# Kernel tuning notes

Measured on AMD Instinct MI355X. Metric: run time of the kernel, lower is better.

Reference implementation:

```python
import jax, jax.numpy as jnp
from jax import lax
import numpy as np

# Config mirroring init_kwargs
B, N, PD = 4, 16384, 3
PROJ = 64                 # projection_channel
M1, K1, C1 = 2048, 32, 128  # level-1 SA: fps points, neighbors, out channel
M2, K2, C2 = 512, 32, 256   # level-2 SA
DH, DO = 512, 256           # dense hidden / out (dense_channels)


def fps(pts, M):
    """Farthest point sampling. pts: [N,3] -> indices [M] (starts at point 0)."""
    n = pts.shape[0]
    def step(carry, _):
        dmin, last = carry
        d = jnp.sum((pts - pts[last]) ** 2, axis=-1)   # dist to newest center
        dmin = jnp.minimum(dmin, d)
        nxt = jnp.argmax(dmin).astype(jnp.int32)
        return (dmin, nxt), last
    init = (jnp.full((n,), 1e10, pts.dtype), jnp.int32(0))
    _, idxs = lax.scan(step, init, None, length=M)
    return idxs


def sa_level(pts, feats, M, K, Wa, ba, Wb, bb):
    """PointNet++ set abstraction: FPS + kNN (xyz space) + grouped MLP + max."""
    idx = jax.vmap(lambda p: fps(p, M))(pts)                       # [B,M]
    centers = jnp.take_along_axis(pts, idx[:, :, None], axis=1)    # [B,M,3]
    d = jnp.sum((centers[:, :, None, :] - pts[:, None, :, :]) ** 2, -1)  # [B,M,N]
    _, nidx = lax.top_k(-d, K)                                      # [B,M,K]
    gather = jax.vmap(lambda a, i: a[i])
    rel = gather(pts, nidx) - centers[:, :, None, :]                # [B,M,K,3]
    nf = gather(feats, nidx)                                        # [B,M,K,C]
    g = jnp.concatenate([rel, nf], axis=-1)                         # use_xyz=True
    h = jax.nn.relu(g @ Wa + ba)
    h = jax.nn.relu(h @ Wb + bb)
    return centers, jnp.max(h, axis=2)                              # [B,M,Cout]


def setup_inputs() -> dict:
    key = jax.random.key(0)
    ks = jax.random.split(key, 12)
    w = lambda k, shape, s: jax.random.normal(k, shape, jnp.float32) * s
    z = lambda c: jnp.zeros((c,), jnp.float32)
    return {
        "xyz": jax.random.normal(ks[0], (B, N, PD), jnp.float32),
        "Wp": w(ks[1], (PD, PROJ), 0.3), "bp": z(PROJ),
        "W1a": w(ks[2], (PROJ + 3, C1), 0.1), "b1a": z(C1),
        "W1b": w(ks[3], (C1, C1), 0.08), "b1b": z(C1),
        "W2a": w(ks[4], (C1 + 3, C2), 0.08), "b2a": z(C2),
        "W2b": w(ks[5], (C2, C2), 0.06), "b2b": z(C2),
        "Wd1": w(ks[6], (2 * C2, DH), 0.05), "bd1": z(DH),
        "Wd2": w(ks[7], (DH, DO), 0.05), "bd2": z(DO),
    }


def reference(xyz, Wp, bp, W1a, b1a, W1b, b1b, W2a, b2a, W2b, b2b,
              Wd1, bd1, Wd2, bd2):
    feats = xyz @ Wp + bp            # point_proj: [B,N,PROJ]
    pts = xyz[..., :3]
    pts, feats = sa_level(pts, feats, M1, K1, W1a, b1a, W1b, b1b)
    pts, feats = sa_level(pts, feats, M2, K2, W2a, b2a, W2b, b2b)
    # global max + avg pool (adaptive_max/avg_pool1d to 1), concat -> [B,2*C2]
    g = jnp.concatenate([jnp.max(feats, axis=1), jnp.mean(feats, axis=1)], -1)
    h = jax.nn.relu(g @ Wd1 + bd1)   # DenseBlock w/ activation
    return h @ Wd2 + bd2             # last block: no activation (last_activation=False)
```

## Files before the change

### kernel.cpp

```cpp
#include <hip/hip_runtime.h>

#define B_    4
#define N1_   16384
#define M1_   2048
#define M2_   512
#define KNN_  32
#define PROJ_ 64
#define C1_   128
#define C2_   256
#define PROJ_OFF_  4
#define TAIL1_OFF_ (PROJ_OFF_ + 8192)
#define TAIL2_OFF_ (TAIL1_OFF_ + 32 * 512)
#define HEAD_OFF_  (TAIL2_OFF_ + 8 * 512)
#define TOTAL_BLKS_ (HEAD_OFF_ + B_)

__device__ __forceinline__ float sqdist_exact(float px, float py, float pz,
                                              float cx, float cy, float cz) {
    float dx = __fsub_rn(px, cx);
    float dy = __fsub_rn(py, cy);
    float dz = __fsub_rn(pz, cz);
    return __fadd_rn(__fadd_rn(__fmul_rn(dx, dx), __fmul_rn(dy, dy)), __fmul_rn(dz, dz));
}

__device__ __forceinline__ float aload(const float* p) {
    return __uint_as_float(__hip_atomic_load((const unsigned*)p,
                           __ATOMIC_RELAXED, __HIP_MEMORY_SCOPE_AGENT));
}
__device__ __forceinline__ unsigned auload(const unsigned* p) {
    return __hip_atomic_load(p, __ATOMIC_RELAXED, __HIP_MEMORY_SCOPE_AGENT);
}
__device__ __forceinline__ void afence() {
    __builtin_amdgcn_fence(__ATOMIC_ACQUIRE, "agent");
}

#define F_PROG1(f,b)  ((f) + (b) * 16)
#define F_PROG2(f,b)  ((f) + 64 + (b) * 16)
#define F_PROJD(f)    ((f) + 128)
#define F_K1D(f,b,c)  ((f) + 192 + ((b) * 32 + (c)) * 16)
#define F_M2D(f,b)    ((f) + 2240 + (b) * 16)
#define F_K2D(f,b,c)  ((f) + 2304 + ((b) * 8 + (c)) * 16)
#define F_M1D(f,b)    ((f) + 2816 + (b) * 16)

__global__ void __launch_bounds__(1024)
sortx_kernel(const float* __restrict__ xyz, float* __restrict__ sx,
             float* __restrict__ sy, float* __restrict__ sz,
             float* __restrict__ sp) {
    const int b = blockIdx.x, t = threadIdx.x;
    const int lane = t & 63, w = t >> 6;
    const float* P = xyz + (size_t)b * N1_ * 3;
    __shared__ int hist[1024];
    __shared__ int wsum[16];
    hist[t] = 0;
    __syncthreads();
    for (int j = t; j < N1_; j += 1024) {
        unsigned kb = __float_as_uint(P[j * 3]);
        kb ^= (kb >> 31) ? 0xFFFFFFFFu : 0x80000000u;
        atomicAdd(&hist[kb >> 22], 1);
    }
    __syncthreads();
    int v = hist[t];
    int cum = v;
    for (int off = 1; off < 64; off <<= 1) {
        int o = __shfl_up(cum, off);
        if (lane >= off) cum += o;
    }
    if (lane == 63) wsum[w] = cum;
    __syncthreads();
    int wpre = 0;
    for (int i = 0; i < w; ++i) wpre += wsum[i];
    const int excl = cum - v + wpre;
    __syncthreads();
    hist[t] = excl;
    __syncthreads();
    for (int j = t; j < N1_; j += 1024) {
        float x = P[j * 3], y = P[j * 3 + 1], z = P[j * 3 + 2];
        unsigned kb = __float_as_uint(x);
        kb ^= (kb >> 31) ? 0xFFFFFFFFu : 0x80000000u;
        int pos = atomicAdd(&hist[kb >> 22], 1);
        size_t o = (size_t)b * N1_ + pos;
        sx[o] = x; sy[o] = y; sz[o] = z;
        float* pr = sp + ((size_t)b * N1_ + pos) * 3;
        pr[0] = x; pr[1] = y; pr[2] = z;
    }
}

typedef float v2f __attribute__((ext_vector_type(2)));

template<int CTRL, int RM>
__device__ __forceinline__ unsigned long long dpp_umax64(unsigned long long pk) {
    unsigned lo = (unsigned)__builtin_amdgcn_update_dpp(
        0, (int)(unsigned)pk, CTRL, RM, 0xf, true);
    unsigned hi = (unsigned)__builtin_amdgcn_update_dpp(
        0, (int)(unsigned)(pk >> 32), CTRL, RM, 0xf, true);
    unsigned long long o = ((unsigned long long)hi << 32) | (unsigned long long)lo;
    return (o > pk) ? o : pk;
}

__device__ __forceinline__ unsigned long long wave_max_key(unsigned long long pk) {
    pk = dpp_umax64<0x111, 0xf>(pk);
    pk = dpp_umax64<0x112, 0xf>(pk);
    pk = dpp_umax64<0x114, 0xf>(pk);
    pk = dpp_umax64<0x118, 0xf>(pk);
    pk = dpp_umax64<0x142, 0xa>(pk);
    pk = dpp_umax64<0x143, 0xc>(pk);
    return pk;
}

__device__ __forceinline__ unsigned reduce8_widx(const unsigned long long* wk,
                                                 int lane) {
    unsigned long long k8 = wk[lane & 7];
    k8 = dpp_umax64<0x111, 0xf>(k8);
    k8 = dpp_umax64<0x112, 0xf>(k8);
    k8 = dpp_umax64<0x114, 0xf>(k8);
    unsigned lo = (unsigned)__builtin_amdgcn_readlane((int)(unsigned)k8, 7);
    return ~lo;
}

template<int N, int NT>
__device__ void knn_bodyT(const float* __restrict__ P,
                          float cx, float cy, float cz,
                          int* __restrict__ out, char* arena) {
    constexpr int K = KNN_;
    constexpr int CAP = 224;
    const int t = threadIdx.x;
    const int lane = t & 63;
    const int w = t >> 6;

    int*      hist = (int*)arena;
    unsigned* eqk  = (unsigned*)(arena + 8192);
    int*      eqi  = (int*)(arena + 8192 + 896);
    int*      wsum = (int*)(arena + 8192 + 1792);
    int*      ctrl = (int*)(arena + 8192 + 1824);

    unsigned prefix = 0; int pbits = 0;
    unsigned Tlo = 0; unsigned long long Thi = 0x100000000ull;
    int L = 0, target = K, Cbin = N;

    for (int round = 0; round < 3; ++round) {
        const int bits  = (round < 2) ? 11 : 10;
        const int nbins = 1 << bits;
        const int shift = 32 - pbits - bits;
        for (int i = t; i < nbins; i += NT) hist[i] = 0;
        __syncthreads();
        for (int j = t; j < N; j += NT) {
            float d = sqdist_exact(P[j * 3], P[j * 3 + 1], P[j * 3 + 2], cx, cy, cz);
            unsigned key = __float_as_uint(d);
            if (key >= Tlo && (unsigned long long)key < Thi)
                atomicAdd(&hist[(key >> shift) & (nbins - 1)], 1);
        }
        __syncthreads();
        const int per = nbins / NT;
        int s = 0;
        for (int i = 0; i < per; ++i) s += hist[t * per + i];
        int cum = s;
        for (int off = 1; off < 64; off <<= 1) {
            int o = __shfl_up(cum, off);
            if (lane >= off) cum += o;
        }
        if (lane == 63) wsum[w] = cum;
        __syncthreads();
        int wpre = 0;
        for (int i = 0; i < w; ++i) wpre += wsum[i];
        cum += wpre;
        const int cumex = cum - s;
        if ((cumex < target) && (cum >= target)) {
            int acc = cumex;
            for (int i = 0; i < per; ++i) {
                int h = hist[t * per + i];
                if (acc + h >= target) { ctrl[2] = t * per + i; ctrl[3] = acc; ctrl[4] = h; break; }
                acc += h;
            }
        }
        __syncthreads();
        const int binsel = ctrl[2];
        const int Ladd   = ctrl[3];
        const int bincnt = ctrl[4];
        L += Ladd;
        target -= Ladd;
        prefix = (prefix << bits) | (unsigned)binsel;
        pbits += bits;
        Tlo = prefix << (32 - pbits);
        Thi = ((unsigned long long)prefix + 1ull) << (32 - pbits);
        Cbin = bincnt;
        __syncthreads();
        if (Cbin <= CAP) break;
    }

    if (t == 0) { ctrl[0] = 0; ctrl[1] = 0; }
    __syncthreads();

    if (Cbin <= CAP) {
        for (int j = t; j < N; j += NT) {
            float d = sqdist_exact(P[j * 3], P[j * 3 + 1], P[j * 3 + 2], cx, cy, cz);
            unsigned key = __float_as_uint(d);
            if (key < Tlo) {
                int p = atomicAdd(&ctrl[0], 1);
                out[p] = j;
            } else if ((unsigned long long)key < Thi) {
                int p = atomicAdd(&ctrl[1], 1);
                eqk[p] = key; eqi[p] = j;
            }
        }
        __syncthreads();
        const int E = ctrl[1];
        for (int e = t; e < E; e += NT) {
            unsigned ke = eqk[e]; int ie = eqi[e];
            int rank = 0;
            for (int f = 0; f < E; ++f) {
                unsigned kf = eqk[f]; int jf = eqi[f];
                rank += (kf < ke || (kf == ke && jf < ie)) ? 1 : 0;
            }
            if (rank < target) out[L + rank] = ie;
        }
    } else {
        if (t < 64) {
            int cnt = 0;
            for (int jb = 0; jb < N; jb += 64) {
                int j = jb + lane;
                float d = sqdist_exact(P[j * 3], P[j * 3 + 1], P[j * 3 + 2], cx, cy, cz);
                unsigned key = __float_as_uint(d);
                if (key < Tlo) {
                    int p = atomicAdd(&ctrl[0], 1);
                    out[p] = j;
                }
                bool eq = (key == Tlo);
                unsigned long long mb = __ballot(eq);
                int below = __popcll(mb & ((1ull << lane) - 1ull));
                if (eq && (cnt + below) < target) out[L + cnt + below] = j;
                cnt += (int)__popcll(mb);
            }
        }
    }
}

__device__ void mlp1_512(int b, int m, char* arena,
                         const float* __restrict__ xyz,
                         const float* __restrict__ feats0,
                         const float* __restrict__ centers1,
                         const int* __restrict__ nidx1,
                         const float* __restrict__ Wa, const float* __restrict__ ba,
                         const float* __restrict__ Wb, const float* __restrict__ bb,
                         float* __restrict__ feats1) {
    constexpr int KN = KNN_, FD = PROJ_, CO = C1_, GS = FD + 4;
    const int t = threadIdx.x;
    const size_t bm = (size_t)b * M1_ + m;
    float (*g)[GS]  = (float(*)[GS])arena;
    float (*h1)[CO] = (float(*)[CO])(arena + 8704);
    float (*pm)[CO] = (float(*)[CO])(arena + 8704 + 16384);
    const int* nb = nidx1 + bm * KN;
    const float* cen = centers1 + bm * 3;
    const float cx = cen[0], cy = cen[1], cz = cen[2];
    {
        const int kk = t >> 4;
        const int q  = t & 15;
        const int j  = nb[kk];
        const float* f = feats0 + ((size_t)b * N1_ + j) * FD + q * 4;
        *(float4*)&g[kk][q * 4] = *(const float4*)f;
        if (q == 0) {
            const float* p = xyz + ((size_t)b * N1_ + j) * 3;
            g[kk][FD + 0] = __fsub_rn(p[0], cx);
            g[kk][FD + 1] = __fsub_rn(p[1], cy);
            g[kk][FD + 2] = __fsub_rn(p[2], cz);
            g[kk][FD + 3] = 0.f;
        }
    }
    __syncthreads();
    const int o = t & (CO - 1);
    const int grp = t >> 7;
    const int k0 = grp * 8;
    float acc[8];
#pragma unroll
    for (int k = 0; k < 8; ++k) acc[k] = ba[o];
    for (int s4 = 0; s4 < FD / 4; ++s4) {
        const float w0 = Wa[(4 * s4 + 3) * CO + o];
        const float w1 = Wa[(4 * s4 + 4) * CO + o];
        const float w2 = Wa[(4 * s4 + 5) * CO + o];
        const float w3 = Wa[(4 * s4 + 6) * CO + o];
#pragma unroll
        for (int k = 0; k < 8; ++k) {
            float4 gv = *(const float4*)&g[k0 + k][4 * s4];
            acc[k] = __fmaf_rn(gv.x, w0, acc[k]);
            acc[k] = __fmaf_rn(gv.y, w1, acc[k]);
            acc[k] = __fmaf_rn(gv.z, w2, acc[k]);
            acc[k] = __fmaf_rn(gv.w, w3, acc[k]);
        }
    }
    {
        const float w0 = Wa[0 * CO + o];
        const float w1 = Wa[1 * CO + o];
        const float w2 = Wa[2 * CO + o];
#pragma unroll
        for (int k = 0; k < 8; ++k) {
            float4 gv = *(const float4*)&g[k0 + k][FD];
            acc[k] = __fmaf_rn(gv.x, w0, acc[k]);
            acc[k] = __fmaf_rn(gv.y, w1, acc[k]);
            acc[k] = __fmaf_rn(gv.z, w2, acc[k]);
        }
    }
#pragma unroll
    for (int k = 0; k < 8; ++k) h1[k0 + k][o] = fmaxf(acc[k], 0.f);
    __syncthreads();
#pragma unroll
    for (int k = 0; k < 8; ++k) acc[k] = bb[o];
    for (int s4 = 0; s4 < CO / 4; ++s4) {
        const float w0 = Wb[(4 * s4 + 0) * CO + o];
        const float w1 = Wb[(4 * s4 + 1) * CO + o];
        const float w2 = Wb[(4 * s4 + 2) * CO + o];
        const float w3 = Wb[(4 * s4 + 3) * CO + o];
#pragma unroll
        for (int k = 0; k < 8; ++k) {
            float4 hv = *(const float4*)&h1[k0 + k][4 * s4];
            acc[k] = __fmaf_rn(hv.x, w0, acc[k]);
            acc[k] = __fmaf_rn(hv.y, w1, acc[k]);
            acc[k] = __fmaf_rn(hv.z, w2, acc[k]);
            acc[k] = __fmaf_rn(hv.w, w3, acc[k]);
        }
    }
    float mx = 0.f;
#pragma unroll
    for (int k = 0; k < 8; ++k) mx = fmaxf(mx, fmaxf(acc[k], 0.f));
    pm[grp][o] = mx;
    __syncthreads();
    if (t < CO) {
        float m0 = fmaxf(fmaxf(pm[0][o], pm[1][o]), fmaxf(pm[2][o], pm[3][o]));
        feats1[bm * CO + o] = m0;
    }
}

__device__ void mlp2_512(int b, int m, char* arena,
                         const float* __restrict__ centers1,
                         const float* __restrict__ feats1,
                         const float* __restrict__ centers2,
                         const int* __restrict__ nidx2,
                         const float* __restrict__ Wa, const float* __restrict__ ba,
                         const float* __restrict__ Wb, const float* __restrict__ bb,
                         float* __restrict__ feats2) {
    constexpr int KN = KNN_, FD = C1_, CO = C2_, GS = FD + 4;
    const int t = threadIdx.x;
    const size_t bm = (size_t)b * M2_ + m;
    float (*g)[GS]  = (float(*)[GS])arena;
    float (*h1)[CO] = (float(*)[CO])(arena + 16896);
    float (*pm)[CO] = (float(*)[CO])(arena + 16896 + 32768);
    const int* nb = nidx2 + bm * KN;
    const float* cen = centers2 + bm * 3;
    const float cx = cen[0], cy = cen[1], cz = cen[2];
    {
        const int kk = t >> 4;
        const int q  = t & 15;
        const int j  = nb[kk];
        const float* f = feats1 + ((size_t)b * M1_ + j) * FD + q * 8;
        *(float4*)&g[kk][q * 8]     = *(const float4*)f;
        *(float4*)&g[kk][q * 8 + 4] = *(const float4*)(f + 4);
        if (q == 0) {
            const float* p = centers1 + ((size_t)b * M1_ + j) * 3;
            g[kk][FD + 0] = __fsub_rn(p[0], cx);
            g[kk][FD + 1] = __fsub_rn(p[1], cy);
            g[kk][FD + 2] = __fsub_rn(p[2], cz);
            g[kk][FD + 3] = 0.f;
        }
    }
    __syncthreads();
    const int o = t & (CO - 1);
    const int grp = t >> 8;
    const int k0 = grp * 16;
    float acc[16];
#pragma unroll
    for (int k = 0; k < 16; ++k) acc[k] = ba[o];
    for (int s4 = 0; s4 < FD / 4; ++s4) {
        const float w0 = Wa[(4 * s4 + 3) * CO + o];
        const float w1 = Wa[(4 * s4 + 4) * CO + o];
        const float w2 = Wa[(4 * s4 + 5) * CO + o];
        const float w3 = Wa[(4 * s4 + 6) * CO + o];
#pragma unroll
        for (int k = 0; k < 16; ++k) {
            float4 gv = *(const float4*)&g[k0 + k][4 * s4];
            acc[k] = __fmaf_rn(gv.x, w0, acc[k]);
            acc[k] = __fmaf_rn(gv.y, w1, acc[k]);
            acc[k] = __fmaf_rn(gv.z, w2, acc[k]);
            acc[k] = __fmaf_rn(gv.w, w3, acc[k]);
        }
    }
    {
        const float w0 = Wa[0 * CO + o];
        const float w1 = Wa[1 * CO + o];
        const float w2 = Wa[2 * CO + o];
#pragma unroll
        for (int k = 0; k < 16; ++k) {
            float4 gv = *(const float4*)&g[k0 + k][FD];
            acc[k] = __fmaf_rn(gv.x, w0, acc[k]);
            acc[k] = __fmaf_rn(gv.y, w1, acc[k]);
            acc[k] = __fmaf_rn(gv.z, w2, acc[k]);
        }
    }
#pragma unroll
    for (int k = 0; k < 16; ++k) h1[k0 + k][o] = fmaxf(acc[k], 0.f);
    __syncthreads();
#pragma unroll
    for (int k = 0; k < 16; ++k) acc[k] = bb[o];
    for (int s4 = 0; s4 < CO / 4; ++s4) {
        const float w0 = Wb[(4 * s4 + 0) * CO + o];
        const float w1 = Wb[(4 * s4 + 1) * CO + o];
        const float w2 = Wb[(4 * s4 + 2) * CO + o];
        const float w3 = Wb[(4 * s4 + 3) * CO + o];
#pragma unroll
        for (int k = 0; k < 16; ++k) {
            float4 hv = *(const float4*)&h1[k0 + k][4 * s4];
            acc[k] = __fmaf_rn(hv.x, w0, acc[k]);
            acc[k] = __fmaf_rn(hv.y, w1, acc[k]);
            acc[k] = __fmaf_rn(hv.z, w2, acc[k]);
            acc[k] = __fmaf_rn(hv.w, w3, acc[k]);
        }
    }
    float mx = 0.f;
#pragma unroll
    for (int k = 0; k < 16; ++k) mx = fmaxf(mx, fmaxf(acc[k], 0.f));
    pm[grp][o] = mx;
    __syncthreads();
    if (t < CO) {
        feats2[bm * CO + o] = fmaxf(pm[0][o], pm[1][o]);
    }
}

__global__ __attribute__((amdgpu_flat_work_group_size(512, 512)))
__attribute__((amdgpu_waves_per_eu(2, 2)))
void mega_kernel(const float* __restrict__ xyz,
                 const float* __restrict__ sx, const float* __restrict__ sy,
                 const float* __restrict__ sz, const float* __restrict__ sp,
                 const float* __restrict__ Wp, const float* __restrict__ bp,
                 const float* __restrict__ W1a, const float* __restrict__ b1a,
                 const float* __restrict__ W1b, const float* __restrict__ b1b,
                 const float* __restrict__ W2a, const float* __restrict__ b2a,
                 const float* __restrict__ W2b, const float* __restrict__ b2b,
                 const float* __restrict__ Wd1, const float* __restrict__ bd1,
                 const float* __restrict__ Wd2, const float* __restrict__ bd2,
                 float* __restrict__ feats0, float* __restrict__ centers1,
                 int* __restrict__ nidx1, float* __restrict__ feats1,
                 float* __restrict__ centers2, int* __restrict__ nidx2,
                 float* __restrict__ feats2, float* __restrict__ outp,
                 unsigned* __restrict__ flags) {
#pragma clang fp contract(off)
    __shared__ alignas(16) char arena[51712];
    asm volatile("" ::: "v255");
    const int bid = blockIdx.x;
    const int t = threadIdx.x;

    if (bid >= HEAD_OFF_) {
        const int b = bid - HEAD_OFF_;
        if (t == 0) {
            while (auload(F_M2D(flags, b)) < (unsigned)M2_)
                __builtin_amdgcn_s_sleep(16);
        }
        __syncthreads();
        afence();
        float* gsh = (float*)arena;
        float* hsh = (float*)(arena + 2048);
        const float* F = feats2 + (size_t)b * M2_ * C2_;
        if (t < C2_) {
            float mx = -1e30f, sm = 0.f;
            for (int r = 0; r < M2_; ++r) {
                float v = F[r * C2_ + t];
                mx = fmaxf(mx, v);
                sm += v;
            }
            gsh[t] = mx;
            gsh[C2_ + t] = sm * (1.0f / (float)M2_);
        }
        __syncthreads();
        if (t < C2_) {
#pragma unroll
            for (int oo = 0; oo < 2; ++oo) {
                const int o = t + oo * 256;
                float acc = bd1[o];
                for (int i = 0; i < 512; ++i)
                    acc = __fmaf_rn(gsh[i], Wd1[i * 512 + o], acc);
                hsh[o] = fmaxf(acc, 0.f);
            }
        }
        __syncthreads();
        if (t < C2_) {
            float acc = bd2[t];
            for (int i = 0; i < 512; ++i)
                acc = __fmaf_rn(hsh[i], Wd2[i * 256 + t], acc);
            outp[b * 256 + t] = acc;
        }
        return;
    }
    if (bid >= TAIL2_OFF_) {
        const int k = bid - TAIL2_OFF_;
        const int c = k >> 9;
        const int r = k & 511;
        const int i = r & 255;
        const int b = (i >> 6) & 3;
        const int m = c * 64 + (i & 63);
        if (r < 256) {
            if (t == 0) {
                while (auload(F_PROG2(flags, b)) <= (unsigned)c)
                    __builtin_amdgcn_s_sleep(16);
            }
            __syncthreads();
            afence();
            const float* cw = centers2 + ((size_t)b * M2_ + m) * 3;
            float cx = cw[0], cy = cw[1], cz = cw[2];
            knn_bodyT<M1_, 512>(centers1 + (size_t)b * M1_ * 3, cx, cy, cz,
                                nidx2 + ((size_t)b * M2_ + m) * KNN_, arena);
            __syncthreads();
            if (t == 0)
                __hip_atomic_fetch_add(F_K2D(flags, b, c), 1u,
                                       __ATOMIC_RELEASE, __HIP_MEMORY_SCOPE_AGENT);
            return;
        }
        if (t == 0) {
            while (auload(F_K2D(flags, b, c)) < 64u ||
                   auload(F_M1D(flags, b)) < (unsigned)M1_)
                __builtin_amdgcn_s_sleep(16);
        }
        __syncthreads();
        afence();
        mlp2_512(b, m, arena, centers1, feats1, centers2, nidx2,
                 W2a, b2a, W2b, b2b, feats2);
        __syncthreads();
        if (t == 0)
            __hip_atomic_fetch_add(F_M2D(flags, b), 1u,
                                   __ATOMIC_RELEASE, __HIP_MEMORY_SCOPE_AGENT);
        return;
    }
    if (bid >= TAIL1_OFF_) {
        const int k = bid - TAIL1_OFF_;
        const int c = k >> 9;
        const int r = k & 511;
        const int i = r & 255;
        const int b = (i >> 6) & 3;
        const int m = c * 64 + (i & 63);
        if (r < 256) {
            if (t == 0) {
                while (auload(F_PROG1(flags, b)) <= (unsigned)c)
                    __builtin_amdgcn_s_sleep(16);
            }
            __syncthreads();
            const float* cw = centers1 + ((size_t)b * M1_ + m) * 3;
            float cx = aload(cw + 0), cy = aload(cw + 1), cz = aload(cw + 2);
            knn_bodyT<N1_, 512>(xyz + (size_t)b * N1_ * 3, cx, cy, cz,
                                nidx1 + ((size_t)b * M1_ + m) * KNN_, arena);
            __syncthreads();
            if (t == 0)
                __hip_atomic_fetch_add(F_K1D(flags, b, c), 1u,
                                       __ATOMIC_RELEASE, __HIP_MEMORY_SCOPE_AGENT);
            return;
        }
        if (t == 0) {
            while (auload(F_K1D(flags, b, c)) < 64u ||
                   auload(F_PROJD(flags)) < 8192u)
                __builtin_amdgcn_s_sleep(16);
        }
        __syncthreads();
        afence();
        mlp1_512(b, m, arena, xyz, feats0, centers1, nidx1,
                 W1a, b1a, W1b, b1b, feats1);
        __syncthreads();
        if (t == 0)
            __hip_atomic_fetch_add(F_M1D(flags, b), 1u,
                                   __ATOMIC_RELEASE, __HIP_MEMORY_SCOPE_AGENT);
        return;
    }
    if (bid >= B_) {
        int tid = (bid - B_) * 512 + t;
        int cc = tid & (PROJ_ - 1);
        int pn = tid >> 6;
        const float* p = xyz + (size_t)pn * 3;
        float acc = p[0] * Wp[0 * PROJ_ + cc];
        acc = __fmaf_rn(p[1], Wp[1 * PROJ_ + cc], acc);
        acc = __fmaf_rn(p[2], Wp[2 * PROJ_ + cc], acc);
        feats0[tid] = acc + bp[cc];
        __syncthreads();
        if (t == 0)
            __hip_atomic_fetch_add(F_PROJD(flags), 1u,
                                   __ATOMIC_RELEASE, __HIP_MEMORY_SCOPE_AGENT);
        return;
    }
    constexpr int NT = 512;
    constexpr int NW = NT / 64;
    const int b = bid;
    const int w = t >> 6;
    const int lane = t & 63;
    const float* P  = xyz + (size_t)b * N1_ * 3;
    const float* SX = sx + (size_t)b * N1_;
    const float* SY = sy + (size_t)b * N1_;
    const float* SZ = sz + (size_t)b * N1_;
    const float* SP = sp + (size_t)b * N1_ * 3;
    float* C1 = centers1 + (size_t)b * M1_ * 3;
    float* C2 = centers2 + (size_t)b * M2_ * 3;

    unsigned long long (*wkey)[NW] = (unsigned long long(*)[NW])arena;
    float* cb1 = (float*)(arena + 128);
    float* cb2 = (float*)(arena + 24704);

    {
        constexpr int PPT = N1_ / NT;
        const int base = t * PPT;
        const unsigned nbase = ~(unsigned)base;

        float px[PPT], py[PPT], pz[PPT], dmin[PPT];
#pragma unroll
        for (int k = 0; k < PPT; ++k) {
            px[k] = SX[base + k];
            py[k] = SY[base + k];
            pz[k] = SZ[base + k];
            dmin[k] = 1e10f;
        }
#pragma unroll
        for (int k = 0; k < PPT; ++k)
            asm volatile("" : "+v"(px[k]), "+v"(py[k]), "+v"(pz[k]), "+v"(dmin[k]));

        float xlo = px[0], xhi = px[0];
#pragma unroll
        for (int k = 1; k < PPT; ++k) {
            xlo = fminf(xlo, px[k]);
            xhi = fmaxf(xhi, px[k]);
        }
        for (int off = 1; off < 64; off <<= 1) {
            xlo = fminf(xlo, __shfl_xor(xlo, off));
            xhi = fmaxf(xhi, __shfl_xor(xhi, off));
        }

        unsigned long long mykey = ((unsigned long long)__float_as_uint(1e10f) << 32);
        float cx = P[0], cy = P[1], cz = P[2];

        for (int m = 0; m < M1_; ++m) {
            if (t == 0) {
                cb1[m * 3 + 0] = cx; cb1[m * 3 + 1] = cy; cb1[m * 3 + 2] = cz;
            }
            if ((m & 63) == 63) {
                __syncthreads();
                const int c = m >> 6;
                if (t < 48)
                    ((float4*)C1)[c * 48 + t] = ((const float4*)cb1)[c * 48 + t];
                __syncthreads();
                if (t == 0)
                    __hip_atomic_store(F_PROG1(flags, b), (unsigned)(c + 1),
                                       __ATOMIC_RELEASE, __HIP_MEMORY_SCOPE_AGENT);
            }
            if (m == M1_ - 1) break;
            const int par = m & 1;
            const float UBval = __uint_as_float((unsigned)(mykey >> 32));
            const float dxs = fmaxf(fmaxf(xlo - cx, cx - xhi), 0.0f);
            if (!(0.999f * (dxs * dxs) >= UBval)) {
                unsigned long long pk = 0;
#pragma unroll
                for (int k = 0; k < PPT; ++k) {
                    float d  = sqdist_exact(px[k], py[k], pz[k], cx, cy, cz);
                    float nd = fminf(dmin[k], d);
                    dmin[k] = nd;
                    unsigned long long kk =
                        ((unsigned long long)__float_as_uint(nd) << 32) |
                        (unsigned)(nbase - (unsigned)k);
                    pk = (kk > pk) ? kk : pk;
                }
                pk = wave_max_key(pk);
                unsigned klo = (unsigned)__builtin_amdgcn_readlane((int)(unsigned)pk, 63);
                unsigned khi = (unsigned)__builtin_amdgcn_readlane((int)(unsigned)(pk >> 32), 63);
                mykey = ((unsigned long long)khi << 32) | klo;
            }
            if (lane == 63) wkey[par][w] = mykey;
            __syncthreads();
            const unsigned widx = reduce8_widx(wkey[par], lane);
            const float* cp = SP + (size_t)widx * 3;
            cx = cp[0]; cy = cp[1]; cz = cp[2];
        }
    }
    __syncthreads();
    {
        constexpr int NP = (M1_ / NT) / 2;
        v2f px2[NP], py2[NP], pz2[NP];
        float dmin[2 * NP];
#pragma unroll
        for (int p = 0; p < NP; ++p) {
            const int j0 = (2 * p) * NT + t;
            const int j1 = j0 + NT;
            px2[p] = (v2f){cb1[j0 * 3 + 0], cb1[j1 * 3 + 0]};
            py2[p] = (v2f){cb1[j0 * 3 + 1], cb1[j1 * 3 + 1]};
            pz2[p] = (v2f){cb1[j0 * 3 + 2], cb1[j1 * 3 + 2]};
            dmin[2 * p] = 1e10f; dmin[2 * p + 1] = 1e10f;
        }
#pragma unroll
        for (int p = 0; p < NP; ++p)
            asm volatile("" : "+v"(px2[p]), "+v"(py2[p]), "+v"(pz2[p]));

        float cx = cb1[0], cy = cb1[1], cz = cb1[2];

        for (int m = 0; m < M2_; ++m) {
            if (t == 0) {
                cb2[m * 3 + 0] = cx; cb2[m * 3 + 1] = cy; cb2[m * 3 + 2] = cz;
            }
            if ((m & 63) == 63) {
                __syncthreads();
                const int c = m >> 6;
                if (t < 48)
                    ((float4*)C2)[c * 48 + t] = ((const float4*)cb2)[c * 48 + t];
                __syncthreads();
                if (t == 0)
                    __hip_atomic_store(F_PROG2(flags, b), (unsigned)(c + 1),
                                       __ATOMIC_RELEASE, __HIP_MEMORY_SCOPE_AGENT);
            }
            if (m == M2_ - 1) break;
            const int par = m & 1;
            const v2f c2x = {cx, cx}, c2y = {cy, cy}, c2z = {cz, cz};
            float bv = -1.0f; int bk = 0;
#pragma unroll
            for (int p = 0; p < NP; ++p) {
                v2f dx = px2[p] - c2x;
                v2f dy = py2[p] - c2y;
                v2f dz = pz2[p] - c2z;
                v2f d2 = (dx * dx + dy * dy) + dz * dz;
                float nd0 = fminf(dmin[2 * p],     d2.x);
                float nd1 = fminf(dmin[2 * p + 1], d2.y);
                dmin[2 * p]     = nd0;
                dmin[2 * p + 1] = nd1;
                bool g0 = nd0 > bv; bv = g0 ? nd0 : bv; bk = g0 ? 2 * p     : bk;
                bool g1 = nd1 > bv; bv = g1 ? nd1 : bv; bk = g1 ? 2 * p + 1 : bk;
            }
            unsigned gi = (unsigned)(bk * NT + t);
            unsigned long long pk =
                ((unsigned long long)__float_as_uint(bv) << 32) | (unsigned)(~gi);
            pk = wave_max_key(pk);
            if (lane == 63) wkey[par][w] = pk;
            __syncthreads();
            const unsigned widx = reduce8_widx(wkey[par], lane);
            cx = cb1[widx * 3 + 0];
            cy = cb1[widx * 3 + 1];
            cz = cb1[widx * 3 + 2];
        }
    }
}

extern "C" void kernel_launch(void* const* d_in, const int* in_sizes, int n_in,
                              void* d_out, int out_size, void* d_ws, size_t ws_size,
                              hipStream_t stream) {
    const float* xyz = (const float*)d_in[0];
    const float* Wp  = (const float*)d_in[1];
    const float* bp  = (const float*)d_in[2];
    const float* W1a = (const float*)d_in[3];
    const float* b1a = (const float*)d_in[4];
    const float* W1b = (const float*)d_in[5];
    const float* b1b = (const float*)d_in[6];
    const float* W2a = (const float*)d_in[7];
    const float* b2a = (const float*)d_in[8];
    const float* W2b = (const float*)d_in[9];
    const float* b2b = (const float*)d_in[10];
    const float* Wd1 = (const float*)d_in[11];
    const float* bd1 = (const float*)d_in[12];
    const float* Wd2 = (const float*)d_in[13];
    const float* bd2 = (const float*)d_in[14];
    float* out = (float*)d_out;

    char* ws = (char*)d_ws;
    size_t off = 0;
    auto alloc = [&](size_t bytes) { void* p = ws + off; off += (bytes + 255) & ~(size_t)255; return p; };
    float* feats0   = (float*)alloc((size_t)B_ * N1_ * PROJ_ * 4);
    float* centers1 = (float*)alloc((size_t)B_ * M1_ * 3 * 4);
    int*   nidx1    = (int*)  alloc((size_t)B_ * M1_ * KNN_ * 4);
    float* feats1   = (float*)alloc((size_t)B_ * M1_ * C1_ * 4);
    float* centers2 = (float*)alloc((size_t)B_ * M2_ * 3 * 4);
    int*   nidx2    = (int*)  alloc((size_t)B_ * M2_ * KNN_ * 4);
    float* feats2   = (float*)alloc((size_t)B_ * M2_ * C2_ * 4);
    unsigned* flags = (unsigned*)alloc(16384);
    float* sx       = (float*)alloc((size_t)B_ * N1_ * 4);
    float* sy       = (float*)alloc((size_t)B_ * N1_ * 4);
    float* sz       = (float*)alloc((size_t)B_ * N1_ * 4);
    float* sp       = (float*)alloc((size_t)B_ * N1_ * 3 * 4);
    (void)in_sizes; (void)n_in; (void)out_size; (void)ws_size;

    hipMemsetAsync(flags, 0, 16384, stream);

    sortx_kernel<<<dim3(B_), dim3(1024), 0, stream>>>(xyz, sx, sy, sz, sp);
    mega_kernel<<<dim3(TOTAL_BLKS_), dim3(512), 0, stream>>>(
        xyz, sx, sy, sz, sp, Wp, bp, W1a, b1a, W1b, b1b,
        W2a, b2a, W2b, b2b, Wd1, bd1, Wd2, bd2,
        feats0, centers1, nidx1, feats1, centers2, nidx2, feats2, out, flags);
}
```

Before: 3.252 ms.

## Split persistent mega-kernel into separate level-1 and level-2 kernels

Breaks the single flag-synchronised mega kernel into one kernel for level-1 FPS, projection, kNN and MLP, and a second kernel for level-2 FPS, kNN, MLP and the dense head. The level-2 FPS now reads centers from global memory after a kernel boundary instead of continuing in the same block from shared memory, and the M1-done flag wait is dropped. Level 1 gets a smaller shared-memory arena, which may allow more resident blocks. The cost is that level-2 FPS can no longer overlap with the level-1 MLP tail, and there is an extra launch.

```diff
diff --git a/kernel.cpp b/kernel.cpp
--- a/kernel.cpp
+++ b/kernel.cpp
@@ -8,11 +8,11 @@
 #define PROJ_ 64
 #define C1_   128
 #define C2_   256
-#define PROJ_OFF_  4
-#define TAIL1_OFF_ (PROJ_OFF_ + 8192)
-#define TAIL2_OFF_ (TAIL1_OFF_ + 32 * 512)
-#define HEAD_OFF_  (TAIL2_OFF_ + 8 * 512)
-#define TOTAL_BLKS_ (HEAD_OFF_ + B_)
+#define PROJ_BLKS_ ((B_ * N1_ * PROJ_) / 512)
+#define TAIL_BLKS_ (32 * 512)
+#define SA2_TAIL_OFF_ 4
+#define SA2_HEAD_OFF_ (SA2_TAIL_OFF_ + 8 * 512)
+#define SA2_BLKS_     (SA2_HEAD_OFF_ + B_)
 
 __device__ __forceinline__ float sqdist_exact(float px, float py, float pz,
                                               float cx, float cy, float cz) {
@@ -39,7 +39,6 @@
 #define F_K1D(f,b,c)  ((f) + 192 + ((b) * 32 + (c)) * 16)
 #define F_M2D(f,b)    ((f) + 2240 + (b) * 16)
 #define F_K2D(f,b,c)  ((f) + 2304 + ((b) * 8 + (c)) * 16)
-#define F_M1D(f,b)    ((f) + 2816 + (b) * 16)
 
 __global__ void __launch_bounds__(1024)
 sortx_kernel(const float* __restrict__ xyz, float* __restrict__ sx,
@@ -423,29 +422,173 @@
 
 __global__ __attribute__((amdgpu_flat_work_group_size(512, 512)))
 __attribute__((amdgpu_waves_per_eu(2, 2)))
-void mega_kernel(const float* __restrict__ xyz,
-                 const float* __restrict__ sx, const float* __restrict__ sy,
-                 const float* __restrict__ sz, const float* __restrict__ sp,
-                 const float* __restrict__ Wp, const float* __restrict__ bp,
-                 const float* __restrict__ W1a, const float* __restrict__ b1a,
-                 const float* __restrict__ W1b, const float* __restrict__ b1b,
-                 const float* __restrict__ W2a, const float* __restrict__ b2a,
-                 const float* __restrict__ W2b, const float* __restrict__ b2b,
-                 const float* __restrict__ Wd1, const float* __restrict__ bd1,
-                 const float* __restrict__ Wd2, const float* __restrict__ bd2,
-                 float* __restrict__ feats0, float* __restrict__ centers1,
-                 int* __restrict__ nidx1, float* __restrict__ feats1,
-                 float* __restrict__ centers2, int* __restrict__ nidx2,
-                 float* __restrict__ feats2, float* __restrict__ outp,
-                 unsigned* __restrict__ flags) {
+void mega1_kernel(const float* __restrict__ xyz,
+                  const float* __restrict__ sx, const float* __restrict__ sy,
+                  const float* __restrict__ sz, const float* __restrict__ sp,
+                  const float* __restrict__ Wp, const float* __restrict__ bp,
+                  const float* __restrict__ W1a, const float* __restrict__ b1a,
+                  const float* __restrict__ W1b, const float* __restrict__ b1b,
+                  float* __restrict__ feats0, float* __restrict__ centers1,
+                  int* __restrict__ nidx1, float* __restrict__ feats1,
+                  unsigned* __restrict__ flags) {
 #pragma clang fp contract(off)
-    __shared__ alignas(16) char arena[51712];
+    __shared__ alignas(16) char arena[27136];
     asm volatile("" ::: "v255");
     const int bid = blockIdx.x;
     const int t = threadIdx.x;
 
-    if (bid >= HEAD_OFF_) {
-        const int b = bid - HEAD_OFF_;
+    if (bid >= B_ + PROJ_BLKS_) {
+        const int k = bid - (B_ + PROJ_BLKS_);
+        const int c = k >> 9;
+        const int r = k & 511;
+        const int i = r & 255;
+        const int b = (i >> 6) & 3;
+        const int m = c * 64 + (i & 63);
+        if (r < 256) {
+            if (t == 0) {
+                while (auload(F_PROG1(flags, b)) <= (unsigned)c)
+                    __builtin_amdgcn_s_sleep(16);
+            }
+            __syncthreads();
+            const float* cw = centers1 + ((size_t)b * M1_ + m) * 3;
+            float cx = aload(cw + 0), cy = aload(cw + 1), cz = aload(cw + 2);
+            knn_bodyT<N1_, 512>(xyz + (size_t)b * N1_ * 3, cx, cy, cz,
+                                nidx1 + ((size_t)b * M1_ + m) * KNN_, arena);
+            __syncthreads();
+            if (t == 0)
+                __hip_atomic_fetch_add(F_K1D(flags, b, c), 1u,
+                                       __ATOMIC_RELEASE, __HIP_MEMORY_SCOPE_AGENT);
+            return;
+        }
+        if (t == 0) {
+            while (auload(F_K1D(flags, b, c)) < 64u ||
+                   auload(F_PROJD(flags)) < (unsigned)PROJ_BLKS_)
+                __builtin_amdgcn_s_sleep(16);
+        }
+        __syncthreads();
+        afence();
+        mlp1_512(b, m, arena, xyz, feats0, centers1, nidx1,
+                 W1a, b1a, W1b, b1b, feats1);
+        return;
+    }
+    if (bid >= B_) {
+        int tid = (bid - B_) * 512 + t;
+        int cc = tid & (PROJ_ - 1);
+        int pn = tid >> 6;
+        const float* p = xyz + (size_t)pn * 3;
+        float acc = p[0] * Wp[0 * PROJ_ + cc];
+        acc = __fmaf_rn(p[1], Wp[1 * PROJ_ + cc], acc);
+        acc = __fmaf_rn(p[2], Wp[2 * PROJ_ + cc], acc);
+        feats0[tid] = acc + bp[cc];
+        __syncthreads();
+        if (t == 0)
+            __hip_atomic_fetch_add(F_PROJD(flags), 1u,
+                                   __ATOMIC_RELEASE, __HIP_MEMORY_SCOPE_AGENT);
+        return;
+    }
+    constexpr int NT = 512;
+    constexpr int NW = NT / 64;
+    constexpr int PPT = N1_ / NT;
+    const int b = bid;
+    const int w = t >> 6;
+    const int lane = t & 63;
+    const float* P  = xyz + (size_t)b * N1_ * 3;
+    const float* SX = sx + (size_t)b * N1_;
+    const float* SY = sy + (size_t)b * N1_;
+    const float* SZ = sz + (size_t)b * N1_;
+    const float* SP = sp + (size_t)b * N1_ * 3;
+    float* C1 = centers1 + (size_t)b * M1_ * 3;
+    const int base = t * PPT;
+    const unsigned nbase = ~(unsigned)base;
+
+    unsigned long long (*wkey)[NW] = (unsigned long long(*)[NW])arena;
+    float* cb1 = (float*)(arena + 128);
+
+    float px[PPT], py[PPT], pz[PPT], dmin[PPT];
+#pragma unroll
+    for (int k = 0; k < PPT; ++k) {
+        px[k] = SX[base + k];
+        py[k] = SY[base + k];
+        pz[k] = SZ[base + k];
+        dmin[k] = 1e10f;
+    }
+#pragma unroll
+    for (int k = 0; k < PPT; ++k)
+        asm volatile("" : "+v"(px[k]), "+v"(py[k]), "+v"(pz[k]), "+v"(dmin[k]));
+
+    float xlo = px[0], xhi = px[0];
+#pragma unroll
+    for (int k = 1; k < PPT; ++k) {
+        xlo = fminf(xlo, px[k]);
+        xhi = fmaxf(xhi, px[k]);
+    }
+    for (int off = 1; off < 64; off <<= 1) {
+        xlo = fminf(xlo, __shfl_xor(xlo, off));
+        xhi = fmaxf(xhi, __shfl_xor(xhi, off));
+    }
+
+    unsigned long long mykey = ((unsigned long long)__float_as_uint(1e10f) << 32);
+    float cx = P[0], cy = P[1], cz = P[2];
+
+    for (int m = 0; m < M1_; ++m) {
+        if (t == 0) {
+            cb1[m * 3 + 0] = cx; cb1[m * 3 + 1] = cy; cb1[m * 3 + 2] = cz;
+        }
+        if ((m & 63) == 63) {
+            __syncthreads();
+            const int c = m >> 6;
+            if (t < 48)
+                ((float4*)C1)[c * 48 + t] = ((const float4*)cb1)[c * 48 + t];
+            __syncthreads();
+            if (t == 0)
+                __hip_atomic_store(F_PROG1(flags, b), (unsigned)(c + 1),
+                                   __ATOMIC_RELEASE, __HIP_MEMORY_SCOPE_AGENT);
+        }
+        if (m == M1_ - 1) break;
+        const int par = m & 1;
+        const float UBval = __uint_as_float((unsigned)(mykey >> 32));
+        const float dxs = fmaxf(fmaxf(xlo - cx, cx - xhi), 0.0f);
+        if (!(0.999f * (dxs * dxs) >= UBval)) {
+            unsigned long long pk = 0;
+#pragma unroll
+            for (int k = 0; k < PPT; ++k) {
+                float d  = sqdist_exact(px[k], py[k], pz[k], cx, cy, cz);
+                float nd = fminf(dmin[k], d);
+                dmin[k] = nd;
+                unsigned long long kk =
+                    ((unsigned long long)__float_as_uint(nd) << 32) |
+                    (unsigned)(nbase - (unsigned)k);
+                pk = (kk > pk) ? kk : pk;
+            }
+            pk = wave_max_key(pk);
+            unsigned klo = (unsigned)__builtin_amdgcn_readlane((int)(unsigned)pk, 63);
+            unsigned khi = (unsigned)__builtin_amdgcn_readlane((int)(unsigned)(pk >> 32), 63);
+            mykey = ((unsigned long long)khi << 32) | klo;
+        }
+        if (lane == 63) wkey[par][w] = mykey;
+        __syncthreads();
+        const unsigned widx = reduce8_widx(wkey[par], lane);
+        const float* cp = SP + (size_t)widx * 3;
+        cx = cp[0]; cy = cp[1]; cz = cp[2];
+    }
+}
+
+__global__ void __launch_bounds__(512)
+sa2_kernel(const float* __restrict__ centers1, const float* __restrict__ feats1,
+           float* __restrict__ centers2, int* __restrict__ nidx2,
+           const float* __restrict__ W2a, const float* __restrict__ b2a,
+           const float* __restrict__ W2b, const float* __restrict__ b2b,
+           const float* __restrict__ Wd1, const float* __restrict__ bd1,
+           const float* __restrict__ Wd2, const float* __restrict__ bd2,
+           float* __restrict__ feats2, float* __restrict__ outp,
+           unsigned* __restrict__ flags) {
+#pragma clang fp contract(off)
+    __shared__ alignas(16) char arena[51712];
+    const int bid = blockIdx.x;
+    const int t = threadIdx.x;
+
+    if (bid >= SA2_HEAD_OFF_) {
+        const int b = bid - SA2_HEAD_OFF_;
         if (t == 0) {
             while (auload(F_M2D(flags, b)) < (unsigned)M2_)
                 __builtin_amdgcn_s_sleep(16);
@@ -485,8 +628,8 @@
         }
         return;
     }
-    if (bid >= TAIL2_OFF_) {
-        const int k = bid - TAIL2_OFF_;
+    if (bid >= SA2_TAIL_OFF_) {
+        const int k = bid - SA2_TAIL_OFF_;
         const int c = k >> 9;
         const int r = k & 511;
         const int i = r & 255;
@@ -510,8 +653,7 @@
             return;
         }
         if (t == 0) {
-            while (auload(F_K2D(flags, b, c)) < 64u ||
-                   auload(F_M1D(flags, b)) < (unsigned)M1_)
+            while (auload(F_K2D(flags, b, c)) < 64u)
                 __builtin_amdgcn_s_sleep(16);
         }
         __syncthreads();
@@ -524,178 +666,45 @@
                                    __ATOMIC_RELEASE, __HIP_MEMORY_SCOPE_AGENT);
         return;
     }
-    if (bid >= TAIL1_OFF_) {
-        const int k = bid - TAIL1_OFF_;
-        const int c = k >> 9;
-        const int r = k & 511;
-        const int i = r & 255;
-        const int b = (i >> 6) & 3;
-        const int m = c * 64 + (i & 63);
-        if (r < 256) {
+    {
+        constexpr int NT = 512;
+        constexpr int NW = 8;
+        constexpr int NP = (M1_ / NT) / 2;
+        const int b = bid;
+        const int w = t >> 6;
+        const int lane = t & 63;
+        const float* P = centers1 + (size_t)b * M1_ * 3;
+        float* C = centers2 + (size_t)b * M2_ * 3;
+
+        unsigned long long (*wkey)[NW] = (unsigned long long(*)[NW])arena;
+        float* cb2 = (float*)(arena + 128);
+
+        v2f px2[NP], py2[NP], pz2[NP];
+        float dmin[2 * NP];
+#pragma unroll
+        for (int p = 0; p < NP; ++p) {
+            const int j0 = (2 * p) * NT + t;
+            const int j1 = j0 + NT;
+            px2[p] = (v2f){P[j0 * 3 + 0], P[j1 * 3 + 0]};
+            py2[p] = (v2f){P[j0 * 3 + 1], P[j1 * 3 + 1]};
+            pz2[p] = (v2f){P[j0 * 3 + 2], P[j1 * 3 + 2]};
+            dmin[2 * p] = 1e10f; dmin[2 * p + 1] = 1e10f;
+        }
+#pragma unroll
+        for (int p = 0; p < NP; ++p)
+            asm volatile("" : "+v"(px2[p]), "+v"(py2[p]), "+v"(pz2[p]));
+
+        float cx = P[0], cy = P[1], cz = P[2];
+
+        for (int m = 0; m < M2_; ++m) {
             if (t == 0) {
-                while (auload(F_PROG1(flags, b)) <= (unsigned)c)
-                    __builtin_amdgcn_s_sleep(16);
-            }
-            __syncthreads();
-            const float* cw = centers1 + ((size_t)b * M1_ + m) * 3;
-            float cx = aload(cw + 0), cy = aload(cw + 1), cz = aload(cw + 2);
-            knn_bodyT<N1_, 512>(xyz + (size_t)b * N1_ * 3, cx, cy, cz,
-                                nidx1 + ((size_t)b * M1_ + m) * KNN_, arena);
-            __syncthreads();
-            if (t == 0)
-                __hip_atomic_fetch_add(F_K1D(flags, b, c), 1u,
-                                       __ATOMIC_RELEASE, __HIP_MEMORY_SCOPE_AGENT);
-            return;
-        }
-        if (t == 0) {
-            while (auload(F_K1D(flags, b, c)) < 64u ||
-                   auload(F_PROJD(flags)) < 8192u)
-                __builtin_amdgcn_s_sleep(16);
-        }
-        __syncthreads();
-        afence();
-        mlp1_512(b, m, arena, xyz, feats0, centers1, nidx1,
-                 W1a, b1a, W1b, b1b, feats1);
-        __syncthreads();
-        if (t == 0)
-            __hip_atomic_fetch_add(F_M1D(flags, b), 1u,
-                                   __ATOMIC_RELEASE, __HIP_MEMORY_SCOPE_AGENT);
-        return;
-    }
-    if (bid >= B_) {
-        int tid = (bid - B_) * 512 + t;
-        int cc = tid & (PROJ_ - 1);
-        int pn = tid >> 6;
-        const float* p = xyz + (size_t)pn * 3;
-        float acc = p[0] * Wp[0 * PROJ_ + cc];
-        acc = __fmaf_rn(p[1], Wp[1 * PROJ_ + cc], acc);
-        acc = __fmaf_rn(p[2], Wp[2 * PROJ_ + cc], acc);
-        feats0[tid] = acc + bp[cc];
-        __syncthreads();
-        if (t == 0)
-            __hip_atomic_fetch_add(F_PROJD(flags), 1u,
-                                   __ATOMIC_RELEASE, __HIP_MEMORY_SCOPE_AGENT);
-        return;
-    }
-    constexpr int NT = 512;
-    constexpr int NW = NT / 64;
-    const int b = bid;
-    const int w = t >> 6;
-    const int lane = t & 63;
-    const float* P  = xyz + (size_t)b * N1_ * 3;
-    const float* SX = sx + (size_t)b * N1_;
-    const float* SY = sy + (size_t)b * N1_;
-    const float* SZ = sz + (size_t)b * N1_;
-    const float* SP = sp + (size_t)b * N1_ * 3;
-    float* C1 = centers1 + (size_t)b * M1_ * 3;
-    float* C2 = centers2 + (size_t)b * M2_ * 3;
-
-    unsigned long long (*wkey)[NW] = (unsigned long long(*)[NW])arena;
-    float* cb1 = (float*)(arena + 128);
-    float* cb2 = (float*)(arena + 24704);
-
-    {
-        constexpr int PPT = N1_ / NT;
-        const int base = t * PPT;
-        const unsigned nbase = ~(unsigned)base;
-
-        float px[PPT], py[PPT], pz[PPT], dmin[PPT];
-#pragma unroll
-        for (int k = 0; k < PPT; ++k) {
-            px[k] = SX[base + k];
-            py[k] = SY[base + k];
-            pz[k] = SZ[base + k];
-            dmin[k] = 1e10f;
-        }
-#pragma unroll
-        for (int k = 0; k < PPT; ++k)
-            asm volatile("" : "+v"(px[k]), "+v"(py[k]), "+v"(pz[k]), "+v"(dmin[k]));
-
-        float xlo = px[0], xhi = px[0];
-#pragma unroll
-        for (int k = 1; k < PPT; ++k) {
-            xlo = fminf(xlo, px[k]);
-            xhi = fmaxf(xhi, px[k]);
-        }
-        for (int off = 1; off < 64; off <<= 1) {
-            xlo = fminf(xlo, __shfl_xor(xlo, off));
-            xhi = fmaxf(xhi, __shfl_xor(xhi, off));
-        }
-
-        unsigned long long mykey = ((unsigned long long)__float_as_uint(1e10f) << 32);
-        float cx = P[0], cy = P[1], cz = P[2];
-
-        for (int m = 0; m < M1_; ++m) {
-            if (t == 0) {
-                cb1[m * 3 + 0] = cx; cb1[m * 3 + 1] = cy; cb1[m * 3 + 2] = cz;
+                cb2[m * 3 + 0] = cx; cb2[m * 3 + 1] = cy; cb2[m * 3 + 2] = cz;
             }
             if ((m & 63) == 63) {
                 __syncthreads();
                 const int c = m >> 6;
                 if (t < 48)
-                    ((float4*)C1)[c * 48 + t] = ((const float4*)cb1)[c * 48 + t];
-                __syncthreads();
-                if (t == 0)
-                    __hip_atomic_store(F_PROG1(flags, b), (unsigned)(c + 1),
-                                       __ATOMIC_RELEASE, __HIP_MEMORY_SCOPE_AGENT);
-            }
-            if (m == M1_ - 1) break;
-            const int par = m & 1;
-            const float UBval = __uint_as_float((unsigned)(mykey >> 32));
-            const float dxs = fmaxf(fmaxf(xlo - cx, cx - xhi), 0.0f);
-            if (!(0.999f * (dxs * dxs) >= UBval)) {
-                unsigned long long pk = 0;
-#pragma unroll
-                for (int k = 0; k < PPT; ++k) {
-                    float d  = sqdist_exact(px[k], py[k], pz[k], cx, cy, cz);
-                    float nd = fminf(dmin[k], d);
-                    dmin[k] = nd;
-                    unsigned long long kk =
-                        ((unsigned long long)__float_as_uint(nd) << 32) |
-                        (unsigned)(nbase - (unsigned)k);
-                    pk = (kk > pk) ? kk : pk;
-                }
-                pk = wave_max_key(pk);
-                unsigned klo = (unsigned)__builtin_amdgcn_readlane((int)(unsigned)pk, 63);
-                unsigned khi = (unsigned)__builtin_amdgcn_readlane((int)(unsigned)(pk >> 32), 63);
-                mykey = ((unsigned long long)khi << 32) | klo;
-            }
-            if (lane == 63) wkey[par][w] = mykey;
-            __syncthreads();
-            const unsigned widx = reduce8_widx(wkey[par], lane);
-            const float* cp = SP + (size_t)widx * 3;
-            cx = cp[0]; cy = cp[1]; cz = cp[2];
-        }
-    }
-    __syncthreads();
-    {
-        constexpr int NP = (M1_ / NT) / 2;
-        v2f px2[NP], py2[NP], pz2[NP];
-        float dmin[2 * NP];
-#pragma unroll
-        for (int p = 0; p < NP; ++p) {
-            const int j0 = (2 * p) * NT + t;
-            const int j1 = j0 + NT;
-            px2[p] = (v2f){cb1[j0 * 3 + 0], cb1[j1 * 3 + 0]};
-            py2[p] = (v2f){cb1[j0 * 3 + 1], cb1[j1 * 3 + 1]};
-            pz2[p] = (v2f){cb1[j0 * 3 + 2], cb1[j1 * 3 + 2]};
-            dmin[2 * p] = 1e10f; dmin[2 * p + 1] = 1e10f;
-        }
-#pragma unroll
-        for (int p = 0; p < NP; ++p)
-            asm volatile("" : "+v"(px2[p]), "+v"(py2[p]), "+v"(pz2[p]));
-
-        float cx = cb1[0], cy = cb1[1], cz = cb1[2];
-
-        for (int m = 0; m < M2_; ++m) {
-            if (t == 0) {
-                cb2[m * 3 + 0] = cx; cb2[m * 3 + 1] = cy; cb2[m * 3 + 2] = cz;
-            }
-            if ((m & 63) == 63) {
-                __syncthreads();
-                const int c = m >> 6;
-                if (t < 48)
-                    ((float4*)C2)[c * 48 + t] = ((const float4*)cb2)[c * 48 + t];
+                    ((float4*)C)[c * 48 + t] = ((const float4*)cb2)[c * 48 + t];
                 __syncthreads();
                 if (t == 0)
                     __hip_atomic_store(F_PROG2(flags, b), (unsigned)(c + 1),
@@ -725,9 +734,8 @@
             if (lane == 63) wkey[par][w] = pk;
             __syncthreads();
             const unsigned widx = reduce8_widx(wkey[par], lane);
-            cx = cb1[widx * 3 + 0];
-            cy = cb1[widx * 3 + 1];
-            cz = cb1[widx * 3 + 2];
+            const float* cp = P + (size_t)widx * 3;
+            cx = cp[0]; cy = cp[1]; cz = cp[2];
         }
     }
 }
@@ -772,8 +780,10 @@
     hipMemsetAsync(flags, 0, 16384, stream);
 
     sortx_kernel<<<dim3(B_), dim3(1024), 0, stream>>>(xyz, sx, sy, sz, sp);
-    mega_kernel<<<dim3(TOTAL_BLKS_), dim3(512), 0, stream>>>(
+    mega1_kernel<<<dim3(B_ + PROJ_BLKS_ + TAIL_BLKS_), dim3(512), 0, stream>>>(
         xyz, sx, sy, sz, sp, Wp, bp, W1a, b1a, W1b, b1b,
-        W2a, b2a, W2b, b2b, Wd1, bd1, Wd2, bd2,
-        feats0, centers1, nidx1, feats1, centers2, nidx2, feats2, out, flags);
-}
+        feats0, centers1, nidx1, feats1, flags);
+    sa2_kernel<<<dim3(SA2_BLKS_), dim3(512), 0, stream>>>(
+        centers1, feats1, centers2, nidx2, W2a, b2a, W2b, b2b,
+        Wd1, bd1, Wd2, bd2, feats2, out, flags);
+}
```

Result: no change. 3.259 ms (+0.2%).
